# Performance work log

Measured on AMD Instinct MI355X. Metric: run time of the kernel, lower is better.

The kernel has to match this reference:

```python
import jax, jax.numpy as jnp
import numpy as np

FACTOR = 2.0
SCALE = 0.2
SOFTMAX_N = 0.0  # softmax_n param; n=0 -> standard softmax

B, H, S, D = 2, 16, 2048, 64


def setup_inputs() -> dict:
    key = jax.random.key(0)
    kq, kk, kv = jax.random.split(key, 3)
    return {
        "query": jax.random.normal(kq, (B, H, S, D), dtype=jnp.float32),
        "key": jax.random.normal(kk, (B, H, S, D), dtype=jnp.float32),
        "value": jax.random.normal(kv, (B, H, S, D), dtype=jnp.float32),
    }


def softmax_n(x, n):
    # exp(x) / (n + sum(exp(x))), numerically stable.
    m = jnp.max(x, axis=-1, keepdims=True)
    e = jnp.exp(x - m)
    denom = n * jnp.exp(-m) + jnp.sum(e, axis=-1, keepdims=True)
    return e / denom


def reference(query, key, value):
    # scores: [B,H,S,S]
    scores = jnp.einsum("bhqd,bhkd->bhqk", query, key) * SCALE
    attn = softmax_n(scores, SOFTMAX_N)
    out = jnp.einsum("bhqk,bhkd->bhqd", attn, value)
    return FACTOR * out
```

## Files before the change

kernel.cpp:

```cpp
#include <hip/hip_runtime.h>
#include <hip/hip_bf16.h>
#include <stdint.h>

typedef __attribute__((ext_vector_type(4))) float f32x4;
typedef __attribute__((ext_vector_type(16))) float f32x16;
typedef __attribute__((ext_vector_type(8))) short s16x8;

__device__ __forceinline__ short f2bf(float f) {
    union { float f; uint32_t u; } v; v.f = f;
    uint32_t r = (v.u + 0x7FFFu + ((v.u >> 16) & 1u)) >> 16;
    return (short)(uint16_t)r;
}

__device__ __forceinline__ uint32_t pk2(float a, float b) {
  union { __hip_bfloat162 h; uint32_t u; } v;
  v.h = __float22bfloat162_rn(make_float2(a, b));
  return v.u;
}

__device__ __forceinline__ void async16(const short* g, short* lds) {
  __builtin_amdgcn_global_load_lds(
      (const __attribute__((address_space(1))) uint32_t*)g,
      (__attribute__((address_space(3))) uint32_t*)lds, 16, 0, 0);
}

__global__ __launch_bounds__(256) void conv_kv_kernel(
    const float* __restrict__ K, const float* __restrict__ V,
    short* __restrict__ Kbf, short* __restrict__ VT) {
  __shared__ short t[64][72];
  const int bh = blockIdx.x >> 5;
  const int st = blockIdx.x & 31;
  const size_t base = (size_t)bh * 131072;

  {
    const int row = threadIdx.x >> 2;
    const int cb = (threadIdx.x & 3) * 16;
    const float* kp = K + base + (size_t)(st * 64 + row) * 64 + cb;
    union { short s[16]; int4 v[2]; } o;
#pragma unroll
    for (int j = 0; j < 16; j += 4) {
      f32x4 a = *(const f32x4*)(kp + j);
#pragma unroll
      for (int q = 0; q < 4; ++q) o.s[j + q] = f2bf(a[q]);
    }
    short* out = Kbf + base + (size_t)(st * 64 + row) * 64 + cb;
    *(int4*)(out) = o.v[0];
    *(int4*)(out + 8) = o.v[1];
  }

  {
    const int s_loc = threadIdx.x >> 2;
    const int dch = (threadIdx.x & 3) * 16;
    const float* p = V + base + (size_t)(st * 64 + s_loc) * 64 + dch;
#pragma unroll
    for (int j = 0; j < 16; j += 4) {
      f32x4 a = *(const f32x4*)(p + j);
#pragma unroll
      for (int q = 0; q < 4; ++q) t[s_loc][dch + j + q] = f2bf(a[q]);
    }
  }
  __syncthreads();
  {
    const int d_loc = threadIdx.x >> 2;
    const int sch = (threadIdx.x & 3) * 16;
    union { short s[16]; int4 v[2]; } o;
#pragma unroll
    for (int i = 0; i < 4; ++i) {
      o.s[i]      = t[sch + i][d_loc];
      o.s[4 + i]  = t[sch + 8 + i][d_loc];
      o.s[8 + i]  = t[sch + 4 + i][d_loc];
      o.s[12 + i] = t[sch + 12 + i][d_loc];
    }
    short* out = VT + base + (size_t)d_loc * 2048 + st * 64 + sch;
    *(int4*)(out) = o.v[0];
    *(int4*)(out + 8) = o.v[1];
  }
}

__global__ __launch_bounds__(256) void attn_fwd_v3(
    const float* __restrict__ Q, const short* __restrict__ Kbf,
    const short* __restrict__ VT, float* __restrict__ O) {
  constexpr int S = 2048, D = 64;
  constexpr int NT = S / 64;
  constexpr float K1 = 0.28853901f;
  constexpr float THR = 11.5415603f;

  __shared__ short kT[2][4096];
  __shared__ short vS[2][4096];

  const int tid = threadIdx.x;
  const int w = tid >> 6;
  const int l = tid & 63;
  const int hi = l >> 5;
  const int c32 = l & 31;

  const int rid = (blockIdx.x & 7) * 64 + (blockIdx.x >> 3);
  const int bh = rid >> 4;
  const int qt = rid & 15;
  const size_t base = (size_t)bh * (size_t)(S * D);
  const int qrow = qt * 128 + w * 32 + c32;

  const short* Kp = Kbf + base;
  const short* Vp = VT + base;

  s16x8 qreg[4];
  {
    const float* qp = Q + base + (size_t)qrow * D;
#pragma unroll
    for (int j = 0; j < 4; ++j) {
      f32x4 a = *(const f32x4*)(qp + j * 16 + hi * 8);
      f32x4 b = *(const f32x4*)(qp + j * 16 + hi * 8 + 4);
      union { uint32_t u[4]; s16x8 v; } pk;
      pk.u[0] = pk2(a[0] * K1, a[1] * K1);
      pk.u[1] = pk2(a[2] * K1, a[3] * K1);
      pk.u[2] = pk2(b[0] * K1, b[1] * K1);
      pk.u[3] = pk2(b[2] * K1, b[3] * K1);
      qreg[j] = pk.v;
    }
  }

  int kSrc[2], vSrc[2], ldsOff[2];
#pragma unroll
  for (int i = 0; i < 2; ++i) {
    const int t = i * 256 + tid;
    const int row = t >> 3, ch = t & 7;
    ldsOff[i] = t * 8;
    kSrc[i] = row * 64 + ((ch ^ (row & 7)) << 3);
    vSrc[i] = row * 2048 + ((ch ^ (row & 7)) << 3);
  }
#define STAGE(buf, kv0)                                       \
  do {                                                        \
    _Pragma("unroll") for (int i = 0; i < 2; ++i) {           \
      async16(Kp + (kv0) * 64 + kSrc[i], &kT[buf][ldsOff[i]]); \
      async16(Vp + (kv0) + vSrc[i], &vS[buf][ldsOff[i]]);      \
    }                                                         \
  } while (0)

  f32x16 o0, o1;
#pragma unroll
  for (int i = 0; i < 16; ++i) { o0[i] = 0.f; o1[i] = 0.f; }
  float m = -1e30f, lsum = 0.f;

  int cur = 0;
  STAGE(0, 0);
  for (int kt = 0; kt < NT; ++kt) {
    __syncthreads();
    if (kt + 1 < NT) STAGE(cur ^ 1, (kt + 1) * 64);
    const char* kB = (const char*)kT[cur];
    const char* vB = (const char*)vS[cur];

#pragma unroll
    for (int grp = 0; grp < 2; ++grp) {
      f32x16 s;
#pragma unroll
      for (int i = 0; i < 16; ++i) s[i] = 0.f;
      const int krow = grp * 32 + c32;
      const int ksw = (krow & 7) << 4;
      __builtin_amdgcn_s_setprio(1);
#pragma unroll
      for (int j = 0; j < 4; ++j) {
        s16x8 a = *(const s16x8*)(kB + krow * 128 + ((j * 32 + hi * 16) ^ ksw));
        s = __builtin_amdgcn_mfma_f32_32x32x16_bf16(a, qreg[j], s, 0, 0, 0);
      }
      __builtin_amdgcn_s_setprio(0);

      float t8[8];
#pragma unroll
      for (int i = 0; i < 8; ++i) t8[i] = fmaxf(s[2 * i], s[2 * i + 1]);
      float t4a = fmaxf(fmaxf(t8[0], t8[1]), fmaxf(t8[2], t8[3]));
      float t4b = fmaxf(fmaxf(t8[4], t8[5]), fmaxf(t8[6], t8[7]));
      float tm = fmaxf(t4a, t4b);
      tm = fmaxf(tm, __shfl_xor(tm, 32));
      if (!__all(tm <= m + THR)) {
        const float mn = fmaxf(m, tm);
        const float scl = exp2f(m - mn);
        lsum *= scl;
        o0 *= scl;
        o1 *= scl;
        m = mn;
      }
      float p[16];
#pragma unroll
      for (int i = 0; i < 16; ++i) p[i] = exp2f(s[i] - m);
      float s8[8];
#pragma unroll
      for (int i = 0; i < 8; ++i) s8[i] = p[2 * i] + p[2 * i + 1];
      float rsa = (s8[0] + s8[1]) + (s8[2] + s8[3]);
      float rsb = (s8[4] + s8[5]) + (s8[6] + s8[7]);
      float rs = rsa + rsb;
      rs += __shfl_xor(rs, 32);
      lsum += rs;

      union { uint32_t u[8]; s16x8 v[2]; } wp;
#pragma unroll
      for (int i = 0; i < 8; ++i) wp.u[i] = pk2(p[2 * i], p[2 * i + 1]);

      __builtin_amdgcn_s_setprio(1);
#pragma unroll
      for (int c = 0; c < 2; ++c) {
        const s16x8 bp = wp.v[c];
        {
          const int vrow = c32;
          s16x8 av = *(const s16x8*)(vB + vrow * 128 +
                                     ((grp * 64 + c * 32 + hi * 16) ^ ((vrow & 7) << 4)));
          o0 = __builtin_amdgcn_mfma_f32_32x32x16_bf16(av, bp, o0, 0, 0, 0);
        }
        {
          const int vrow = 32 + c32;
          s16x8 av = *(const s16x8*)(vB + vrow * 128 +
                                     ((grp * 64 + c * 32 + hi * 16) ^ ((vrow & 7) << 4)));
          o1 = __builtin_amdgcn_mfma_f32_32x32x16_bf16(av, bp, o1, 0, 0, 0);
        }
      }
      __builtin_amdgcn_s_setprio(0);
    }
    cur ^= 1;
  }
#undef STAGE

  const float f = 2.0f / lsum;
  float* op = O + base + (size_t)qrow * D;
#pragma unroll
  for (int rq = 0; rq < 4; ++rq) {
    const int d0 = rq * 8 + 4 * hi;
    f32x4 v0, v1;
#pragma unroll
    for (int i = 0; i < 4; ++i) {
      v0[i] = o0[rq * 4 + i] * f;
      v1[i] = o1[rq * 4 + i] * f;
    }
    *(f32x4*)(op + d0) = v0;
    *(f32x4*)(op + d0 + 32) = v1;
  }
}

__global__ __launch_bounds__(256) void attn_fwd_v1(
    const float* __restrict__ Q, const float* __restrict__ K,
    const float* __restrict__ V, float* __restrict__ O) {
  constexpr int S = 2048, D = 64;
  constexpr float SCALE = 0.2f, FACTOR = 2.0f;
  constexpr int KVBLK = 64, NT = S / KVBLK;
  __shared__ short kT[64 * 64];
  __shared__ short vT[64 * 64];
  __shared__ short pT[4][16 * 64];
  const int tid = threadIdx.x;
  const int w = tid >> 6, l = tid & 63, g = l >> 4, c = l & 15;
  const int bh = blockIdx.x >> 5, qt = blockIdx.x & 31;
  const size_t base = (size_t)bh * (size_t)(S * D);
  char* kB = (char*)kT; char* vB = (char*)vT; char* pB = (char*)pT[w];
  s16x8 qa[2];
  {
    const float* qp = Q + base + (size_t)(qt * 64 + w * 16 + c) * D + g * 8;
#pragma unroll
    for (int kk = 0; kk < 2; ++kk) {
      f32x4 q0 = *(const f32x4*)(qp + kk * 32);
      f32x4 q1 = *(const f32x4*)(qp + kk * 32 + 4);
      s16x8 a;
#pragma unroll
      for (int i = 0; i < 4; ++i) { a[i] = f2bf(q0[i]); a[4 + i] = f2bf(q1[i]); }
      qa[kk] = a;
    }
  }
  f32x4 o_acc[4];
#pragma unroll
  for (int nb = 0; nb < 4; ++nb) o_acc[nb] = (f32x4){0.f, 0.f, 0.f, 0.f};
  float m_r[4], l_r[4];
#pragma unroll
  for (int r = 0; r < 4; ++r) { m_r[r] = -1e30f; l_r[r] = 0.f; }
  const int krow = tid >> 2, kcb = tid & 3;
  const int vpr = (tid >> 3) * 2, vpc = (tid & 7) * 8;
  for (int kt = 0; kt < NT; ++kt) {
    const int kv0 = kt * KVBLK;
    __syncthreads();
    {
      const float* kp = K + base + (size_t)(kv0 + krow) * D + kcb * 16;
      f32x4 a0 = *(const f32x4*)(kp);
      f32x4 a1 = *(const f32x4*)(kp + 4);
      f32x4 a2 = *(const f32x4*)(kp + 8);
      f32x4 a3 = *(const f32x4*)(kp + 12);
      union { short s[8]; int4 v; } p0, p1;
#pragma unroll
      for (int i = 0; i < 4; ++i) {
        p0.s[i] = f2bf(a0[i]); p0.s[4 + i] = f2bf(a1[i]);
        p1.s[i] = f2bf(a2[i]); p1.s[4 + i] = f2bf(a3[i]);
      }
      const int sw = (krow & 7) << 4;
      *(int4*)(kB + krow * 128 + ((kcb * 32) ^ sw)) = p0.v;
      *(int4*)(kB + krow * 128 + ((kcb * 32 + 16) ^ sw)) = p1.v;
    }
    {
      const float* vp = V + base + (size_t)(kv0 + vpr) * D + vpc;
      f32x4 r0a = *(const f32x4*)(vp);
      f32x4 r0b = *(const f32x4*)(vp + 4);
      f32x4 r1a = *(const f32x4*)(vp + D);
      f32x4 r1b = *(const f32x4*)(vp + D + 4);
      float lo[8] = {r0a[0], r0a[1], r0a[2], r0a[3], r0b[0], r0b[1], r0b[2], r0b[3]};
      float hi2[8] = {r1a[0], r1a[1], r1a[2], r1a[3], r1b[0], r1b[1], r1b[2], r1b[3]};
#pragma unroll
      for (int i = 0; i < 8; ++i) {
        uint32_t pk = (uint32_t)(uint16_t)f2bf(lo[i]) |
                      ((uint32_t)(uint16_t)f2bf(hi2[i]) << 16);
        const int col = vpc + i;
        *(uint32_t*)(vB + col * 128 + ((vpr * 2) ^ ((col & 7) << 4))) = pk;
      }
    }
    __syncthreads();
    f32x4 sc[4];
#pragma unroll
    for (int nb = 0; nb < 4; ++nb) sc[nb] = (f32x4){0.f, 0.f, 0.f, 0.f};
#pragma unroll
    for (int kk = 0; kk < 2; ++kk) {
#pragma unroll
      for (int nb = 0; nb < 4; ++nb) {
        const int row = nb * 16 + c;
        s16x8 b = *(const s16x8*)(kB + row * 128 +
                                  ((kk * 64 + g * 16) ^ ((row & 7) << 4)));
        sc[nb] = __builtin_amdgcn_mfma_f32_16x16x32_bf16(qa[kk], b, sc[nb], 0, 0, 0);
      }
    }
    float p[4][4]; float esc[4];
#pragma unroll
    for (int r = 0; r < 4; ++r) {
      float mx = fmaxf(fmaxf(sc[0][r], sc[1][r]), fmaxf(sc[2][r], sc[3][r]));
#pragma unroll
      for (int mask = 1; mask < 16; mask <<= 1)
        mx = fmaxf(mx, __shfl_xor(mx, mask, 64));
      mx *= SCALE;
      const float mnew = fmaxf(m_r[r], mx);
      esc[r] = __expf(m_r[r] - mnew);
      float rs = 0.f;
#pragma unroll
      for (int nb = 0; nb < 4; ++nb) {
        float e = __expf(sc[nb][r] * SCALE - mnew);
        p[nb][r] = e; rs += e;
      }
#pragma unroll
      for (int mask = 1; mask < 16; mask <<= 1)
        rs += __shfl_xor(rs, mask, 64);
      l_r[r] = l_r[r] * esc[r] + rs;
      m_r[r] = mnew;
    }
#pragma unroll
    for (int nb = 0; nb < 4; ++nb)
#pragma unroll
      for (int r = 0; r < 4; ++r) o_acc[nb][r] *= esc[r];
#pragma unroll
    for (int nb = 0; nb < 4; ++nb) {
#pragma unroll
      for (int r = 0; r < 4; ++r) {
        const int row = 4 * g + r;
        const int colb = (nb * 16 + c) * 2;
        *(short*)(pB + row * 128 + (colb ^ ((row & 7) << 4))) = f2bf(p[nb][r]);
      }
    }
    asm volatile("s_waitcnt lgkmcnt(0)" ::: "memory");
#pragma unroll
    for (int kk = 0; kk < 2; ++kk) {
      s16x8 pa = *(const s16x8*)(pB + c * 128 +
                                 ((kk * 64 + g * 16) ^ ((c & 7) << 4)));
#pragma unroll
      for (int nb = 0; nb < 4; ++nb) {
        const int row = nb * 16 + c;
        s16x8 vb = *(const s16x8*)(vB + row * 128 +
                                   ((kk * 64 + g * 16) ^ ((row & 7) << 4)));
        o_acc[nb] = __builtin_amdgcn_mfma_f32_16x16x32_bf16(pa, vb, o_acc[nb], 0, 0, 0);
      }
    }
  }
#pragma unroll
  for (int r = 0; r < 4; ++r) {
    const float f = FACTOR / l_r[r];
    const size_t rowg = (size_t)(qt * 64 + w * 16 + 4 * g + r);
    float* op = O + base + rowg * D + c;
#pragma unroll
    for (int nb = 0; nb < 4; ++nb) op[nb * 16] = o_acc[nb][r] * f;
  }
}

extern "C" void kernel_launch(void* const* d_in, const int* in_sizes, int n_in,
                              void* d_out, int out_size, void* d_ws, size_t ws_size,
                              hipStream_t stream) {
  (void)in_sizes; (void)n_in; (void)out_size;
  const float* Q = (const float*)d_in[0];
  const float* K = (const float*)d_in[1];
  const float* V = (const float*)d_in[2];
  float* O = (float*)d_out;
  constexpr size_t NEED = 2ull * 2 * 16 * 2048 * 64 * sizeof(short);
  if (ws_size >= NEED && d_ws) {
    short* Kbf = (short*)d_ws;
    short* VT = Kbf + 2 * 16 * 2048 * 64;
    hipLaunchKernelGGL(conv_kv_kernel, dim3(1024), dim3(256), 0, stream, K, V, Kbf, VT);
    hipLaunchKernelGGL(attn_fwd_v3, dim3(512), dim3(256), 0, stream, Q, Kbf, VT, O);
  } else {
    hipLaunchKernelGGL(attn_fwd_v1, dim3(1024), dim3(256), 0, stream, Q, K, V, O);
  }
}
```

Before: 169.5 us.

## Split KV sequence across warp pairs with in-block softmax merge

Each block now covers 64 query rows instead of 128. Its four waves form two query halves times two KV halves, and each wave walks half the key sequence in 32-row tiles. Partial max, sum and output accumulators are then merged through LDS at the end. The grid doubles to 1024 blocks to improve occupancy and load balance across CUs. The cost is more K/V traffic per query row, an extra combine step with LDS writes, and a new V staging layout with different swizzling.

```diff
diff --git a/kernel.cpp b/kernel.cpp
--- a/kernel.cpp
+++ b/kernel.cpp
@@ -77,28 +77,29 @@
   }
 }
 
-__global__ __launch_bounds__(256) void attn_fwd_v3(
+__global__ __launch_bounds__(256) void attn_fwd_v4(
     const float* __restrict__ Q, const short* __restrict__ Kbf,
     const short* __restrict__ VT, float* __restrict__ O) {
   constexpr int S = 2048, D = 64;
-  constexpr int NT = S / 64;
+  constexpr int NT = 32;
   constexpr float K1 = 0.28853901f;
   constexpr float THR = 11.5415603f;
 
-  __shared__ short kT[2][4096];
-  __shared__ short vS[2][4096];
+  __shared__ short lds_s[16384];
 
   const int tid = threadIdx.x;
   const int w = tid >> 6;
   const int l = tid & 63;
   const int hi = l >> 5;
   const int c32 = l & 31;
-
-  const int rid = (blockIdx.x & 7) * 64 + (blockIdx.x >> 3);
-  const int bh = rid >> 4;
-  const int qt = rid & 15;
+  const int qhalf = w & 1;
+  const int kvhalf = w >> 1;
+
+  const int rid = (blockIdx.x & 7) * 128 + (blockIdx.x >> 3);
+  const int bh = rid >> 5;
+  const int qt = rid & 31;
   const size_t base = (size_t)bh * (size_t)(S * D);
-  const int qrow = qt * 128 + w * 32 + c32;
+  const int qrow = qt * 64 + qhalf * 32 + c32;
 
   const short* Kp = Kbf + base;
   const short* Vp = VT + base;
@@ -119,21 +120,22 @@
     }
   }
 
-  int kSrc[2], vSrc[2], ldsOff[2];
-#pragma unroll
-  for (int i = 0; i < 2; ++i) {
-    const int t = i * 256 + tid;
-    const int row = t >> 3, ch = t & 7;
-    ldsOff[i] = t * 8;
-    kSrc[i] = row * 64 + ((ch ^ (row & 7)) << 3);
-    vSrc[i] = row * 2048 + ((ch ^ (row & 7)) << 3);
-  }
-#define STAGE(buf, kv0)                                       \
-  do {                                                        \
-    _Pragma("unroll") for (int i = 0; i < 2; ++i) {           \
-      async16(Kp + (kv0) * 64 + kSrc[i], &kT[buf][ldsOff[i]]); \
-      async16(Vp + (kv0) + vSrc[i], &vS[buf][ldsOff[i]]);      \
-    }                                                         \
+  const int rS = tid >> 3, chS = tid & 7;
+  const int kSrcOff = rS * 64 + ((chS ^ (rS & 7)) << 3);
+  const int dV = 2 * rS + (chS >> 2);
+  const int vSrcOff = dV * 2048 + (((chS & 3) ^ (rS & 3)) << 3);
+  const int ldsOff = tid * 8;
+
+  short* kS0 = lds_s;
+  short* vS0 = lds_s + 8192;
+
+#define STAGE(buf, kt)                                                    \
+  do {                                                                    \
+    _Pragma("unroll") for (int h = 0; h < 2; ++h) {                       \
+      const int kv0 = h * 1024 + (kt) * 32;                               \
+      async16(Kp + kv0 * 64 + kSrcOff, kS0 + ((buf)*2 + h) * 2048 + ldsOff); \
+      async16(Vp + kv0 + vSrcOff, vS0 + ((buf)*2 + h) * 2048 + ldsOff);   \
+    }                                                                     \
   } while (0)
 
   f32x16 o0, o1;
@@ -145,92 +147,106 @@
   STAGE(0, 0);
   for (int kt = 0; kt < NT; ++kt) {
     __syncthreads();
-    if (kt + 1 < NT) STAGE(cur ^ 1, (kt + 1) * 64);
-    const char* kB = (const char*)kT[cur];
-    const char* vB = (const char*)vS[cur];
-
-#pragma unroll
-    for (int grp = 0; grp < 2; ++grp) {
-      f32x16 s;
-#pragma unroll
-      for (int i = 0; i < 16; ++i) s[i] = 0.f;
-      const int krow = grp * 32 + c32;
-      const int ksw = (krow & 7) << 4;
-      __builtin_amdgcn_s_setprio(1);
-#pragma unroll
-      for (int j = 0; j < 4; ++j) {
-        s16x8 a = *(const s16x8*)(kB + krow * 128 + ((j * 32 + hi * 16) ^ ksw));
-        s = __builtin_amdgcn_mfma_f32_32x32x16_bf16(a, qreg[j], s, 0, 0, 0);
-      }
-      __builtin_amdgcn_s_setprio(0);
-
-      float t8[8];
-#pragma unroll
-      for (int i = 0; i < 8; ++i) t8[i] = fmaxf(s[2 * i], s[2 * i + 1]);
-      float t4a = fmaxf(fmaxf(t8[0], t8[1]), fmaxf(t8[2], t8[3]));
-      float t4b = fmaxf(fmaxf(t8[4], t8[5]), fmaxf(t8[6], t8[7]));
-      float tm = fmaxf(t4a, t4b);
-      tm = fmaxf(tm, __shfl_xor(tm, 32));
-      if (!__all(tm <= m + THR)) {
-        const float mn = fmaxf(m, tm);
-        const float scl = exp2f(m - mn);
-        lsum *= scl;
-        o0 *= scl;
-        o1 *= scl;
-        m = mn;
-      }
-      float p[16];
-#pragma unroll
-      for (int i = 0; i < 16; ++i) p[i] = exp2f(s[i] - m);
-      float s8[8];
-#pragma unroll
-      for (int i = 0; i < 8; ++i) s8[i] = p[2 * i] + p[2 * i + 1];
-      float rsa = (s8[0] + s8[1]) + (s8[2] + s8[3]);
-      float rsb = (s8[4] + s8[5]) + (s8[6] + s8[7]);
-      float rs = rsa + rsb;
-      rs += __shfl_xor(rs, 32);
-      lsum += rs;
-
-      union { uint32_t u[8]; s16x8 v[2]; } wp;
-#pragma unroll
-      for (int i = 0; i < 8; ++i) wp.u[i] = pk2(p[2 * i], p[2 * i + 1]);
-
-      __builtin_amdgcn_s_setprio(1);
-#pragma unroll
-      for (int c = 0; c < 2; ++c) {
-        const s16x8 bp = wp.v[c];
-        {
-          const int vrow = c32;
-          s16x8 av = *(const s16x8*)(vB + vrow * 128 +
-                                     ((grp * 64 + c * 32 + hi * 16) ^ ((vrow & 7) << 4)));
-          o0 = __builtin_amdgcn_mfma_f32_32x32x16_bf16(av, bp, o0, 0, 0, 0);
-        }
-        {
-          const int vrow = 32 + c32;
-          s16x8 av = *(const s16x8*)(vB + vrow * 128 +
-                                     ((grp * 64 + c * 32 + hi * 16) ^ ((vrow & 7) << 4)));
-          o1 = __builtin_amdgcn_mfma_f32_32x32x16_bf16(av, bp, o1, 0, 0, 0);
-        }
-      }
-      __builtin_amdgcn_s_setprio(0);
-    }
+    if (kt + 1 < NT) STAGE(cur ^ 1, kt + 1);
+    const char* kB = (const char*)(kS0 + (cur * 2 + kvhalf) * 2048);
+    const char* vB = (const char*)(vS0 + (cur * 2 + kvhalf) * 2048);
+
+    f32x16 s;
+#pragma unroll
+    for (int i = 0; i < 16; ++i) s[i] = 0.f;
+    const int ksw = (c32 & 7) << 4;
+    __builtin_amdgcn_s_setprio(1);
+#pragma unroll
+    for (int j = 0; j < 4; ++j) {
+      s16x8 a = *(const s16x8*)(kB + c32 * 128 + ((j * 32 + hi * 16) ^ ksw));
+      s = __builtin_amdgcn_mfma_f32_32x32x16_bf16(a, qreg[j], s, 0, 0, 0);
+    }
+    __builtin_amdgcn_s_setprio(0);
+
+    float t8[8];
+#pragma unroll
+    for (int i = 0; i < 8; ++i) t8[i] = fmaxf(s[2 * i], s[2 * i + 1]);
+    float t4a = fmaxf(fmaxf(t8[0], t8[1]), fmaxf(t8[2], t8[3]));
+    float t4b = fmaxf(fmaxf(t8[4], t8[5]), fmaxf(t8[6], t8[7]));
+    float tm = fmaxf(t4a, t4b);
+    tm = fmaxf(tm, __shfl_xor(tm, 32));
+    if (!__all(tm <= m + THR)) {
+      const float mn = fmaxf(m, tm);
+      const float scl = exp2f(m - mn);
+      lsum *= scl;
+      o0 *= scl;
+      o1 *= scl;
+      m = mn;
+    }
+    float p[16];
+#pragma unroll
+    for (int i = 0; i < 16; ++i) p[i] = exp2f(s[i] - m);
+    float s8[8];
+#pragma unroll
+    for (int i = 0; i < 8; ++i) s8[i] = p[2 * i] + p[2 * i + 1];
+    float rs = ((s8[0] + s8[1]) + (s8[2] + s8[3])) +
+               ((s8[4] + s8[5]) + (s8[6] + s8[7]));
+    rs += __shfl_xor(rs, 32);
+    lsum += rs;
+
+    union { uint32_t u[8]; s16x8 v[2]; } wp;
+#pragma unroll
+    for (int i = 0; i < 8; ++i) wp.u[i] = pk2(p[2 * i], p[2 * i + 1]);
+
+    __builtin_amdgcn_s_setprio(1);
+#pragma unroll
+    for (int c = 0; c < 2; ++c) {
+      const s16x8 bp = wp.v[c];
+      {
+        const int d = c32;
+        const int r = d >> 1;
+        s16x8 av = *(const s16x8*)(vB + r * 128 + (d & 1) * 64 +
+                                   (((c * 2 + hi) ^ (r & 3)) << 4));
+        o0 = __builtin_amdgcn_mfma_f32_32x32x16_bf16(av, bp, o0, 0, 0, 0);
+      }
+      {
+        const int d = 32 + c32;
+        const int r = d >> 1;
+        s16x8 av = *(const s16x8*)(vB + r * 128 + (d & 1) * 64 +
+                                   (((c * 2 + hi) ^ (r & 3)) << 4));
+        o1 = __builtin_amdgcn_mfma_f32_32x32x16_bf16(av, bp, o1, 0, 0, 0);
+      }
+    }
+    __builtin_amdgcn_s_setprio(0);
     cur ^= 1;
   }
 #undef STAGE
 
-  const float f = 2.0f / lsum;
-  float* op = O + base + (size_t)qrow * D;
-#pragma unroll
-  for (int rq = 0; rq < 4; ++rq) {
-    const int d0 = rq * 8 + 4 * hi;
-    f32x4 v0, v1;
-#pragma unroll
-    for (int i = 0; i < 4; ++i) {
-      v0[i] = o0[rq * 4 + i] * f;
-      v1[i] = o1[rq * 4 + i] * f;
-    }
-    *(f32x4*)(op + d0) = v0;
-    *(f32x4*)(op + d0 + 32) = v1;
+  __syncthreads();
+  float* comb = (float*)lds_s;
+  if (kvhalf == 1) {
+    float* dst = comb + (qhalf * 64 + l) * 36;
+    dst[0] = m;
+    dst[1] = lsum;
+#pragma unroll
+    for (int i = 0; i < 16; ++i) { dst[2 + i] = o0[i]; dst[18 + i] = o1[i]; }
+  }
+  __syncthreads();
+  if (kvhalf == 0) {
+    const float* src = comb + (qhalf * 64 + l) * 36;
+    const float mb = src[0], lb = src[1];
+    const float mm = fmaxf(m, mb);
+    const float a = exp2f(m - mm);
+    const float b = exp2f(mb - mm);
+    const float f = 2.0f / (lsum * a + lb * b);
+    float* op = O + base + (size_t)qrow * D;
+#pragma unroll
+    for (int rq = 0; rq < 4; ++rq) {
+      const int d0 = rq * 8 + 4 * hi;
+      f32x4 v0, v1;
+#pragma unroll
+      for (int i = 0; i < 4; ++i) {
+        v0[i] = (o0[rq * 4 + i] * a + src[2 + rq * 4 + i] * b) * f;
+        v1[i] = (o1[rq * 4 + i] * a + src[18 + rq * 4 + i] * b) * f;
+      }
+      *(f32x4*)(op + d0) = v0;
+      *(f32x4*)(op + d0 + 32) = v1;
+    }
   }
 }
 
@@ -390,7 +406,7 @@
     short* Kbf = (short*)d_ws;
     short* VT = Kbf + 2 * 16 * 2048 * 64;
     hipLaunchKernelGGL(conv_kv_kernel, dim3(1024), dim3(256), 0, stream, K, V, Kbf, VT);
-    hipLaunchKernelGGL(attn_fwd_v3, dim3(512), dim3(256), 0, stream, Q, Kbf, VT, O);
+    hipLaunchKernelGGL(attn_fwd_v4, dim3(1024), dim3(256), 0, stream, Q, Kbf, VT, O);
   } else {
     hipLaunchKernelGGL(attn_fwd_v1, dim3(1024), dim3(256), 0, stream, Q, K, V, O);
   }
```

New measurement: 165.1 us. -2.6%, faster.
